# Kernel tuning notes

Measured on AMD Instinct MI355X. Metric: run time of the kernel, lower is better.

## Reference

```python
import jax, jax.numpy as jnp
import numpy as np

T, B, H, V = 128, 32, 1024, 32000


def setup_inputs() -> dict:
    key = jax.random.key(0)
    ks = jax.random.split(key, 8)
    scale = 1.0 / np.sqrt(H)
    return {
        "input": jax.random.normal(ks[0], (T, B, H), dtype=jnp.float32),
        "hidden": jnp.zeros((B, H), dtype=jnp.float32),
        "w_ic": jax.random.uniform(ks[1], (H, H), jnp.float32, -scale, scale),
        "w_ix": jax.random.uniform(ks[2], (H, H), jnp.float32, -scale, scale),
        "w_fc": jax.random.uniform(ks[3], (H, H), jnp.float32, -scale, scale),
        "w_fx": jax.random.uniform(ks[4], (H, H), jnp.float32, -scale, scale),
        "b_i": jnp.zeros((H,), dtype=jnp.float32),
        "b_f": jnp.zeros((H,), dtype=jnp.float32),
        "W_out": jax.random.uniform(ks[5], (V, H), jnp.float32, -scale, scale),
        "b_out": jnp.zeros((V,), dtype=jnp.float32),
    }


def reference(input, hidden, w_ic, w_ix, w_fc, w_fx, b_i, b_f, W_out, b_out):
    # Precompute input projections for all timesteps: [T, B, H]
    ix = jnp.einsum("tbh,kh->tbk", input, w_ix)
    fx = jnp.einsum("tbh,kh->tbk", input, w_fx)

    def step(c, xs):
        ix_t, fx_t, x_t = xs
        i_t = jax.nn.sigmoid(c @ w_ic.T + b_i + ix_t)
        f_t = jax.nn.sigmoid(c @ w_fc.T + b_f + fx_t)
        c_new = i_t * x_t + f_t * c  # RAN gated-additive update
        return c_new, c_new

    hidden_final, outputs = jax.lax.scan(step, hidden, (ix, fx, input))
    logits = jnp.einsum("tbh,vh->tbv", outputs, W_out) + b_out
    log_probs = jax.nn.log_softmax(logits, axis=-1)
    return log_probs, hidden_final
```

## Files before the change

kernel.cpp:

```cpp
#include <hip/hip_runtime.h>

typedef __attribute__((ext_vector_type(4))) float f32x4;
typedef __attribute__((ext_vector_type(8))) short bf16x8;
typedef __attribute__((ext_vector_type(4))) unsigned u32x4;

#define T_DIM 128
#define B_DIM 32
#define H_DIM 1024
#define V_DIM 32000
#define MROWS 4096
#define NBLK 64
#define CSTEP 32768
#define PUBSTEP 32768
#define WSTRIDE 1028

__device__ __forceinline__ ushort f2bf(float f){
  union { float f; unsigned u; } x; x.f = f;
  unsigned u = x.u;
  unsigned r = (u + 0x7fffu + ((u >> 16) & 1u)) >> 16;
  return (ushort)r;
}
__device__ __forceinline__ float bf2f(ushort h){
  union { unsigned u; float f; } x; x.u = ((unsigned)h) << 16;
  return x.f;
}

__device__ __forceinline__ void async_copy16(void* lds, const void* g){
  __builtin_amdgcn_global_load_lds((const __attribute__((address_space(1))) void*)g,
                                   (__attribute__((address_space(3))) void*)lds, 16, 0, 0);
}

__global__ void cast_bf16_kernel(const float* __restrict__ s, ushort* __restrict__ d, int n4){
  int stride = gridDim.x * blockDim.x;
  for (int i = blockIdx.x*blockDim.x + threadIdx.x; i < n4; i += stride){
    float4 v = ((const float4*)s)[i];
    ushort4 o = make_ushort4(f2bf(v.x), f2bf(v.y), f2bf(v.z), f2bf(v.w));
    ((ushort4*)d)[i] = o;
  }
}

__global__ void cast_split_kernel(const float* __restrict__ s, ushort* __restrict__ dh,
                                  ushort* __restrict__ dl, int n4){
  int stride = gridDim.x * blockDim.x;
  for (int i = blockIdx.x*blockDim.x + threadIdx.x; i < n4; i += stride){
    float4 v = ((const float4*)s)[i];
    ushort4 h = make_ushort4(f2bf(v.x), f2bf(v.y), f2bf(v.z), f2bf(v.w));
    ushort4 l = make_ushort4(f2bf(v.x - bf2f(h.x)), f2bf(v.y - bf2f(h.y)),
                             f2bf(v.z - bf2f(h.z)), f2bf(v.w - bf2f(h.w)));
    ((ushort4*)dh)[i] = h;
    ((ushort4*)dl)[i] = l;
  }
}

__global__ __launch_bounds__(256) void gemm_bt(
    const ushort* __restrict__ A, const ushort* __restrict__ B,
    float* __restrict__ C, const float* __restrict__ bias,
    int N, int K, int NTN, int order, int achunk,
    float* __restrict__ pmax, float* __restrict__ psum)
{
  __shared__ ushort lA[128*32];
  __shared__ ushort lB[128*32];
  __shared__ float pmS[4][64], psS[4][64];
  int tid = threadIdx.x;
  int lane = tid & 63, wid = tid >> 6;
  int bid = blockIdx.x;
  int tm, tn;
  if (order){
    int xcd = bid & 7, id = bid >> 3;
    tn = id >> 2;
    tm = (xcd << 2) | (id & 3);
  } else {
    tm = bid / NTN; tn = bid % NTN;
  }
  int row0 = tm << 7, col0 = tn << 7;

  f32x4 acc[4][4] = {};

  auto stage = [&](const ushort* __restrict__ g, ushort* l, int r0, int k0){
    int c = wid << 1;
    const ushort* s0 = g + (size_t)(r0 + (c<<4) + (lane>>2))*K + k0 + ((lane&3)<<3);
    async_copy16(l + (c<<9), s0);
    async_copy16(l + ((c+1)<<9), s0 + (size_t)16*K);
  };
  auto stageAc = [&](const ushort* __restrict__ g, ushort* l, int r0, int k0){
    int c = wid << 1;
    int cb  = (k0 >> 4) + ((lane & 3) >> 1);
    int sub = (lane & 1) << 3;
    int rA = r0 + (c<<4) + (lane>>2);
    const ushort* sA = g + ((size_t)(rA>>5)<<15) + (cb<<9) + ((rA&31)<<4) + sub;
    async_copy16(l + (c<<9), sA);
    int rB = rA + 16;
    const ushort* sB = g + ((size_t)(rB>>5)<<15) + (cb<<9) + ((rB&31)<<4) + sub;
    async_copy16(l + ((c+1)<<9), sB);
  };

  int nk = K >> 5;
  if (achunk) stageAc(A, lA, row0, 0); else stage(A, lA, row0, 0);
  stage(B, lB, col0, 0);
  int wm = (wid >> 1) << 6, wn = (wid & 1) << 6;
  int kg = (lane >> 4) << 3;
  int ar = lane & 15;

  for (int kt = 0; kt < nk; ++kt){
    __syncthreads();
    bf16x8 af[4], bfr[4];
    #pragma unroll
    for (int mi = 0; mi < 4; ++mi) af[mi]  = *(const bf16x8*)&lA[(wm + mi*16 + ar)*32 + kg];
    #pragma unroll
    for (int ni = 0; ni < 4; ++ni) bfr[ni] = *(const bf16x8*)&lB[(wn + ni*16 + ar)*32 + kg];
    #pragma unroll
    for (int mi = 0; mi < 4; ++mi)
      #pragma unroll
      for (int ni = 0; ni < 4; ++ni)
        acc[mi][ni] = __builtin_amdgcn_mfma_f32_16x16x32_bf16(af[mi], bfr[ni], acc[mi][ni], 0, 0, 0);
    if (kt + 1 < nk){
      __syncthreads();
      if (achunk) stageAc(A, lA, row0, (kt+1) << 5); else stage(A, lA, row0, (kt+1) << 5);
      stage(B, lB, col0, (kt+1) << 5);
    }
  }

  int rr = (lane >> 4) << 2;
  float bb4[4];
  #pragma unroll
  for (int ni = 0; ni < 4; ++ni) bb4[ni] = bias ? bias[col0 + wn + ni*16 + ar] : 0.f;

  #pragma unroll
  for (int mi = 0; mi < 4; ++mi){
    #pragma unroll
    for (int q = 0; q < 4; ++q){
      int r = row0 + wm + mi*16 + rr + q;
      float vals[4];
      #pragma unroll
      for (int ni = 0; ni < 4; ++ni){
        vals[ni] = acc[mi][ni][q] + bb4[ni];
        C[(size_t)r * N + col0 + wn + ni*16 + ar] = vals[ni];
      }
      if (pmax){
        float m = fmaxf(fmaxf(vals[0], vals[1]), fmaxf(vals[2], vals[3]));
        #pragma unroll
        for (int o = 1; o < 16; o <<= 1) m = fmaxf(m, __shfl_xor(m, o));
        float s = expf(vals[0]-m) + expf(vals[1]-m) + expf(vals[2]-m) + expf(vals[3]-m);
        #pragma unroll
        for (int o = 1; o < 16; o <<= 1) s += __shfl_xor(s, o);
        if (ar == 0){ int rl = mi*16 + rr + q; pmS[wid][rl] = m; psS[wid][rl] = s; }
      }
    }
  }
  if (pmax){
    __syncthreads();
    if (tid < 128){
      int rl = tid & 63, half = tid >> 6;
      int w0 = half*2, w1 = w0 + 1;
      float m0 = pmS[w0][rl], m1 = pmS[w1][rl];
      float s0 = psS[w0][rl], s1 = psS[w1][rl];
      float M = fmaxf(m0, m1);
      float S = s0*expf(m0-M) + s1*expf(m1-M);
      int r = row0 + half*64 + rl;
      pmax[(size_t)r*NTN + tn] = M;
      psum[(size_t)r*NTN + tn] = S;
    }
  }
}

__global__ __launch_bounds__(256) void gemm_bt_split(
    const ushort* __restrict__ Ah, const ushort* __restrict__ Al,
    const ushort* __restrict__ Bh, const ushort* __restrict__ Bl,
    float* __restrict__ C, int N, int K, int NTN)
{
  __shared__ ushort lAh[128*32], lAl[128*32], lBh[128*32], lBl[128*32];
  int tid = threadIdx.x;
  int lane = tid & 63, wid = tid >> 6;
  int tm = blockIdx.x / NTN, tn = blockIdx.x % NTN;
  int row0 = tm << 7, col0 = tn << 7;

  f32x4 acc[4][4] = {};

  auto stage = [&](const ushort* __restrict__ g, ushort* l, int r0, int k0){
    int c = wid << 1;
    const ushort* s0 = g + (size_t)(r0 + (c<<4) + (lane>>2))*K + k0 + ((lane&3)<<3);
    async_copy16(l + (c<<9), s0);
    async_copy16(l + ((c+1)<<9), s0 + (size_t)16*K);
  };

  int nk = K >> 5;
  stage(Ah, lAh, row0, 0); stage(Al, lAl, row0, 0);
  stage(Bh, lBh, col0, 0); stage(Bl, lBl, col0, 0);
  int wm = (wid >> 1) << 6, wn = (wid & 1) << 6;
  int kg = (lane >> 4) << 3;
  int ar = lane & 15;

  for (int kt = 0; kt < nk; ++kt){
    __syncthreads();
    bf16x8 afh[4], afl[4], bfh[4], bfl[4];
    #pragma unroll
    for (int mi = 0; mi < 4; ++mi){
      afh[mi] = *(const bf16x8*)&lAh[(wm + mi*16 + ar)*32 + kg];
      afl[mi] = *(const bf16x8*)&lAl[(wm + mi*16 + ar)*32 + kg];
    }
    #pragma unroll
    for (int ni = 0; ni < 4; ++ni){
      bfh[ni] = *(const bf16x8*)&lBh[(wn + ni*16 + ar)*32 + kg];
      bfl[ni] = *(const bf16x8*)&lBl[(wn + ni*16 + ar)*32 + kg];
    }
    #pragma unroll
    for (int mi = 0; mi < 4; ++mi)
      #pragma unroll
      for (int ni = 0; ni < 4; ++ni){
        acc[mi][ni] = __builtin_amdgcn_mfma_f32_16x16x32_bf16(afh[mi], bfh[ni], acc[mi][ni], 0, 0, 0);
        acc[mi][ni] = __builtin_amdgcn_mfma_f32_16x16x32_bf16(afh[mi], bfl[ni], acc[mi][ni], 0, 0, 0);
        acc[mi][ni] = __builtin_amdgcn_mfma_f32_16x16x32_bf16(afl[mi], bfh[ni], acc[mi][ni], 0, 0, 0);
      }
    if (kt + 1 < nk){
      __syncthreads();
      stage(Ah, lAh, row0, (kt+1) << 5); stage(Al, lAl, row0, (kt+1) << 5);
      stage(Bh, lBh, col0, (kt+1) << 5); stage(Bl, lBl, col0, (kt+1) << 5);
    }
  }

  int rr = (lane >> 4) << 2;
  #pragma unroll
  for (int mi = 0; mi < 4; ++mi)
    #pragma unroll
    for (int ni = 0; ni < 4; ++ni){
      int r  = row0 + wm + mi*16 + rr;
      int cc = col0 + wn + ni*16 + ar;
      #pragma unroll
      for (int q = 0; q < 4; ++q)
        C[(size_t)(r + q) * N + cc] = acc[mi][ni][q];
    }
}

__global__ __launch_bounds__(512) void ran_all(
    unsigned* __restrict__ pub, const float* __restrict__ hiddenf,
    const ushort* __restrict__ wh, const ushort* __restrict__ wl,
    const float* __restrict__ b_i, const float* __restrict__ b_f,
    const float* __restrict__ ixfx, const float* __restrict__ x_all,
    float* __restrict__ hid_final)
{
  __shared__ ushort lWh[32*WSTRIDE];
  __shared__ ushort lWl[32*WSTRIDE];
  __shared__ f32x4 part[4][2][2][64];
  __shared__ float gsm[2*32*17];
  __shared__ float cfl[32][17];

  int tid = threadIdx.x, lane = tid & 63, wid = tid >> 6;
  int kq = wid & 3, mh = wid >> 2;
  int rgate = wid & 1, rmh = (wid >> 1) & 1;
  int bid = blockIdx.x;
  int nb = bid << 4;
  int ar = lane & 15, kg = (lane >> 4) << 3;
  int um = tid >> 4, uk = tid & 15;

  #pragma unroll
  for (int u = 0; u < 8; ++u){
    int unit = u*512 + tid;
    int r = unit >> 7, off = (unit & 127) << 3;
    int g = r >> 4, c = r & 15;
    size_t gsrc = (size_t)((g<<10) + nb + c) * H_DIM + off;
    *(bf16x8*)&lWh[r*WSTRIDE + off] = *(const bf16x8*)&wh[gsrc];
    *(bf16x8*)&lWl[r*WSTRIDE + off] = *(const bf16x8*)&wl[gsrc];
  }
  cfl[um][uk] = hiddenf[(um<<10) + nb + uk];
  float bb = (rgate ? b_f : b_i)[nb + ar];
  const ushort* b0h = &lWh[(     ar)*WSTRIDE + (kq<<8) + kg];
  const ushort* b0l = &lWl[(     ar)*WSTRIDE + (kq<<8) + kg];
  const ushort* b1h = &lWh[(16 + ar)*WSTRIDE + (kq<<8) + kg];
  const ushort* b1l = &lWl[(16 + ar)*WSTRIDE + (kq<<8) + kg];
  int abase = (kq<<13) + ((kg>>4)<<9) + (((mh<<4) + ar)<<4) + (kg & 8);
  __syncthreads();

  for (int t = 0; t < T_DIM; ++t){
    float xq1 = x_all[((size_t)t<<15) + (um<<10) + nb + uk];
    float pix[4];
    if (wid < 4){
      const float* ix_t = ixfx + ((size_t)t<<16);
      #pragma unroll
      for (int q = 0; q < 4; ++q){
        int m = (rmh<<4) + ((lane>>4)<<2) + q;
        pix[q] = ix_t[m*2048 + (rgate<<10) + nb + ar];
      }
    }

    const unsigned* ps = pub + ((size_t)t << 15) + abase;
    unsigned expt = (unsigned)(t + 1) << 16;
    u32x4 w0[8], w1[8];
    int tries = 0;
    while (1){
      #pragma unroll
      for (int f = 0; f < 8; ++f){
        const unsigned* p = ps + (f << 10);
        asm volatile("global_load_dwordx4 %0, %2, off sc0 sc1\n\t"
                     "global_load_dwordx4 %1, %2, off offset:16 sc0 sc1"
                     : "=&v"(w0[f]), "=&v"(w1[f]) : "v"(p));
      }
      asm volatile("s_waitcnt vmcnt(0)" ::: "memory");
      __builtin_amdgcn_sched_barrier(0);
      unsigned bad = 0;
      #pragma unroll
      for (int f = 0; f < 8; ++f){
        bad |= (w0[f][0]^expt)|(w0[f][1]^expt)|(w0[f][2]^expt)|(w0[f][3]^expt)
             | (w1[f][0]^expt)|(w1[f][1]^expt)|(w1[f][2]^expt)|(w1[f][3]^expt);
      }
      if (__ballot((bad & 0xFFFF0000u) != 0) == 0ull) break;
      if (++tries > (1<<15)) break;
    }

    f32x4 g0h = {}, g0l = {}, g1h = {}, g1l = {};
    #pragma unroll
    for (int f = 0; f < 8; ++f){
      union { unsigned u[4]; bf16x8 v; } cv;
      cv.u[0] = (w0[f][0] & 0xFFFFu) | (w0[f][1] << 16);
      cv.u[1] = (w0[f][2] & 0xFFFFu) | (w0[f][3] << 16);
      cv.u[2] = (w1[f][0] & 0xFFFFu) | (w1[f][1] << 16);
      cv.u[3] = (w1[f][2] & 0xFFFFu) | (w1[f][3] << 16);
      int ob = f << 5;
      bf16x8 v0h = *(const bf16x8*)&b0h[ob];
      bf16x8 v0l = *(const bf16x8*)&b0l[ob];
      bf16x8 v1h = *(const bf16x8*)&b1h[ob];
      bf16x8 v1l = *(const bf16x8*)&b1l[ob];
      g0h = __builtin_amdgcn_mfma_f32_16x16x32_bf16(cv.v, v0h, g0h, 0, 0, 0);
      g0l = __builtin_amdgcn_mfma_f32_16x16x32_bf16(cv.v, v0l, g0l, 0, 0, 0);
      g1h = __builtin_amdgcn_mfma_f32_16x16x32_bf16(cv.v, v1h, g1h, 0, 0, 0);
      g1l = __builtin_amdgcn_mfma_f32_16x16x32_bf16(cv.v, v1l, g1l, 0, 0, 0);
    }
    part[kq][mh][0][lane] = g0h + g0l;
    part[kq][mh][1][lane] = g1h + g1l;
    __syncthreads();

    if (wid < 4){
      f32x4 sum = part[0][rmh][rgate][lane] + part[1][rmh][rgate][lane]
                + part[2][rmh][rgate][lane] + part[3][rmh][rgate][lane];
      #pragma unroll
      for (int q = 0; q < 4; ++q){
        int m = (rmh<<4) + ((lane>>4)<<2) + q;
        float pre = sum[q] + bb + pix[q];
        gsm[((rgate<<5) + m)*17 + ar] = 1.f / (1.f + expf(-pre));
      }
    }
    __syncthreads();

    {
      float iv = gsm[um*17 + uk];
      float fv = gsm[(32+um)*17 + uk];
      float cv2 = cfl[um][uk];
      float cn = iv * xq1 + fv * cv2;
      cfl[um][uk] = cn;
      unsigned word = ((unsigned)(t + 2) << 16) | (unsigned)f2bf(cn);
      __hip_atomic_store(&pub[((size_t)(t+1) << 15) + (bid << 9) + tid], word,
                         __ATOMIC_RELAXED, __HIP_MEMORY_SCOPE_AGENT);
      if (t == T_DIM-1) hid_final[(um<<10) + nb + uk] = cn;
    }
    __syncthreads();
  }
}

__global__ void init_c_kernel(const float* __restrict__ hidden, unsigned* __restrict__ pub){
  int i = blockIdx.x * blockDim.x + threadIdx.x;
  float v = hidden[i];
  int m = i >> 10, col = i & 1023;
  pub[((col>>4)<<9) + (m<<4) + (col&15)] = (1u << 16) | (unsigned)f2bf(v);
}

__global__ void untag_kernel(const unsigned* __restrict__ pub, ushort* __restrict__ cst){
  int e = (blockIdx.x * blockDim.x + threadIdx.x) << 2;
  int s = e >> 15, w = e & 32767;
  const unsigned* p = pub + ((size_t)(s + 1) << 15) + w;
  ushort4 o = make_ushort4((ushort)p[0], (ushort)p[1], (ushort)p[2], (ushort)p[3]);
  *(ushort4*)&cst[e] = o;
}

__global__ __launch_bounds__(64) void lse_reduce(const float* __restrict__ pmax,
                                                 const float* __restrict__ psum,
                                                 float* __restrict__ lse, int ntn){
  int row = blockIdx.x, lane = threadIdx.x;
  float m = -1e30f, s = 0.f;
  for (int i = lane; i < ntn; i += 64){
    float mi = pmax[(size_t)row*ntn + i], si = psum[(size_t)row*ntn + i];
    float M = fmaxf(m, mi);
    s = s*expf(m - M) + si*expf(mi - M);
    m = M;
  }
  #pragma unroll
  for (int o = 32; o; o >>= 1){
    float m2 = __shfl_xor(m, o), s2 = __shfl_xor(s, o);
    float M = fmaxf(m, m2);
    s = s*expf(m - M) + s2*expf(m2 - M);
    m = M;
  }
  if (lane == 0) lse[row] = m + logf(s);
}

__global__ __launch_bounds__(256) void sub_kernel(float* __restrict__ logits,
                                                  const float* __restrict__ lse){
  size_t row = blockIdx.x;
  float l = lse[row];
  float4* p4 = (float4*)(logits + row * (size_t)V_DIM);
  for (int i = threadIdx.x; i < V_DIM/4; i += 256){
    float4 v = p4[i];
    v.x -= l; v.y -= l; v.z -= l; v.w -= l;
    p4[i] = v;
  }
}

extern "C" void kernel_launch(void* const* d_in, const int* in_sizes, int n_in,
                              void* d_out, int out_size, void* d_ws, size_t ws_size,
                              hipStream_t stream)
{
  const float* input  = (const float*)d_in[0];
  const float* hidden = (const float*)d_in[1];
  const float* w_ic   = (const float*)d_in[2];
  const float* w_ix   = (const float*)d_in[3];
  const float* w_fc   = (const float*)d_in[4];
  const float* w_fx   = (const float*)d_in[5];
  const float* b_i    = (const float*)d_in[6];
  const float* b_f    = (const float*)d_in[7];
  const float* W_out  = (const float*)d_in[8];
  const float* b_out  = (const float*)d_in[9];
  float* out = (float*)d_out;

  char* ws = (char*)d_ws;
  ushort* wout_bf = (ushort*)(ws + 0);
  ushort* in_hi   = (ushort*)(ws + 65536000);
  ushort* in_lo   = (ushort*)(ws + 73924608);
  ushort* wx_hi   = (ushort*)(ws + 82313216);
  ushort* wx_lo   = (ushort*)(ws + 86507520);
  ushort* wc_hi   = (ushort*)(ws + 90701824);
  ushort* wc_lo   = (ushort*)(ws + 94896128);
  unsigned* pub   = (unsigned*)(ws + 65536000);
  ushort* cstate  = (ushort*)(ws + 82444288);
  float*  pmax    = (float*)(ws + 94896128);
  float*  psum    = (float*)(ws + 99090432);
  float*  lse     = (float*)(ws + 103186432);
  float*  ixfx    = out;

  cast_bf16_kernel <<<2048,256,0,stream>>>(W_out, wout_bf, V_DIM*H_DIM/4);
  cast_split_kernel<<<1024,256,0,stream>>>(input, in_hi, in_lo, MROWS*H_DIM/4);
  cast_split_kernel<<<256,256,0,stream>>>(w_ix, wx_hi,             wx_lo,             H_DIM*H_DIM/4);
  cast_split_kernel<<<256,256,0,stream>>>(w_fx, wx_hi+H_DIM*H_DIM, wx_lo+H_DIM*H_DIM, H_DIM*H_DIM/4);
  cast_split_kernel<<<256,256,0,stream>>>(w_ic, wc_hi,             wc_lo,             H_DIM*H_DIM/4);
  cast_split_kernel<<<256,256,0,stream>>>(w_fc, wc_hi+H_DIM*H_DIM, wc_lo+H_DIM*H_DIM, H_DIM*H_DIM/4);

  gemm_bt_split<<<32*16,256,0,stream>>>(in_hi, in_lo, wx_hi, wx_lo, ixfx, 2048, H_DIM, 16);

  hipMemsetAsync(pub, 0, (size_t)129 * PUBSTEP * 4, stream);
  init_c_kernel<<<128,256,0,stream>>>(hidden, pub);

  ran_all<<<NBLK,512,0,stream>>>(pub, hidden, wc_hi, wc_lo, b_i, b_f,
                                 ixfx, input, out + (size_t)MROWS*V_DIM);

  untag_kernel<<<4096,256,0,stream>>>(pub, cstate);
  gemm_bt<<<32*250,256,0,stream>>>(cstate, wout_bf, out, b_out, V_DIM, H_DIM, 250, 1, 1, pmax, psum);
  lse_reduce<<<MROWS,64,0,stream>>>(pmax, psum, lse, 250);
  sub_kernel<<<MROWS,256,0,stream>>>(out, lse);
}
```

Baseline: 1.999 ms.

## Replace output projection GEMM with 256x256 double-buffered swizzled LDS kernel

The vocabulary projection GEMM moves from 128x128 tiles with single-buffered K=32 stages to 256x256 tiles with 512 threads, K=64 stages, double-buffered async LDS loads, and XOR-swizzled LDS layout to avoid bank conflicts. This raises arithmetic intensity per byte loaded and overlaps global loads with MFMA work. The partial softmax max/sum is reduced across four column waves, and the LSE reduction now covers 125 partials. The larger tile uses much more LDS (about 128KB), which limits occupancy to one block per CU. Tile edges depend on V being divisible by 256, which holds for 32000.

```diff
diff --git a/kernel.cpp b/kernel.cpp
--- a/kernel.cpp
+++ b/kernel.cpp
@@ -10,7 +10,6 @@
 #define V_DIM 32000
 #define MROWS 4096
 #define NBLK 64
-#define CSTEP 32768
 #define PUBSTEP 32768
 #define WSTRIDE 1028
 
@@ -52,114 +51,119 @@
   }
 }
 
-__global__ __launch_bounds__(256) void gemm_bt(
+__global__ __launch_bounds__(512) void gemm256(
     const ushort* __restrict__ A, const ushort* __restrict__ B,
     float* __restrict__ C, const float* __restrict__ bias,
-    int N, int K, int NTN, int order, int achunk,
     float* __restrict__ pmax, float* __restrict__ psum)
 {
-  __shared__ ushort lA[128*32];
-  __shared__ ushort lB[128*32];
-  __shared__ float pmS[4][64], psS[4][64];
-  int tid = threadIdx.x;
-  int lane = tid & 63, wid = tid >> 6;
+  __shared__ ushort lA[2][256*64];
+  __shared__ ushort lB[2][256*64];
+  __shared__ float redm[2][4][128], reds[2][4][128];
+
+  const int K = 1024, N = V_DIM, NTN = 125, NT = 16;
+  int tid = threadIdx.x, lane = tid & 63, wid = tid >> 6;
+  int wm = wid >> 2, wn = wid & 3;
   int bid = blockIdx.x;
-  int tm, tn;
-  if (order){
-    int xcd = bid & 7, id = bid >> 3;
-    tn = id >> 2;
-    tm = (xcd << 2) | (id & 3);
-  } else {
-    tm = bid / NTN; tn = bid % NTN;
-  }
-  int row0 = tm << 7, col0 = tn << 7;
-
-  f32x4 acc[4][4] = {};
-
-  auto stage = [&](const ushort* __restrict__ g, ushort* l, int r0, int k0){
-    int c = wid << 1;
-    const ushort* s0 = g + (size_t)(r0 + (c<<4) + (lane>>2))*K + k0 + ((lane&3)<<3);
-    async_copy16(l + (c<<9), s0);
-    async_copy16(l + ((c+1)<<9), s0 + (size_t)16*K);
+  int xcd = bid & 7, id = bid >> 3;
+  int tm = (xcd << 1) | (id & 1);
+  int tn = id >> 1;
+  int row0 = tm << 8, col0 = tn << 8;
+  int ar = lane & 15, kg = (lane >> 4) << 3;
+
+  auto STAGE = [&](int buf, int k0){
+    #pragma unroll
+    for (int j = 0; j < 4; ++j){
+      int l16 = j*512 + tid;
+      int row = l16 >> 3, g = l16 & 7;
+      int kc = (g ^ (row & 7)) << 3;
+      int rA = row0 + row, k = k0 + kc;
+      const ushort* sA = A + ((size_t)(rA>>5)<<15) + ((k>>4)<<9) + ((rA&31)<<4) + (k&15);
+      async_copy16(&lA[buf][l16<<3], sA);
+    }
+    #pragma unroll
+    for (int j = 0; j < 4; ++j){
+      int l16 = j*512 + tid;
+      int row = l16 >> 3, g = l16 & 7;
+      int kc = (g ^ (row & 7)) << 3;
+      const ushort* sB = B + (size_t)(col0 + row)*K + k0 + kc;
+      async_copy16(&lB[buf][l16<<3], sB);
+    }
   };
-  auto stageAc = [&](const ushort* __restrict__ g, ushort* l, int r0, int k0){
-    int c = wid << 1;
-    int cb  = (k0 >> 4) + ((lane & 3) >> 1);
-    int sub = (lane & 1) << 3;
-    int rA = r0 + (c<<4) + (lane>>2);
-    const ushort* sA = g + ((size_t)(rA>>5)<<15) + (cb<<9) + ((rA&31)<<4) + sub;
-    async_copy16(l + (c<<9), sA);
-    int rB = rA + 16;
-    const ushort* sB = g + ((size_t)(rB>>5)<<15) + (cb<<9) + ((rB&31)<<4) + sub;
-    async_copy16(l + ((c+1)<<9), sB);
-  };
-
-  int nk = K >> 5;
-  if (achunk) stageAc(A, lA, row0, 0); else stage(A, lA, row0, 0);
-  stage(B, lB, col0, 0);
-  int wm = (wid >> 1) << 6, wn = (wid & 1) << 6;
-  int kg = (lane >> 4) << 3;
-  int ar = lane & 15;
-
-  for (int kt = 0; kt < nk; ++kt){
-    __syncthreads();
-    bf16x8 af[4], bfr[4];
-    #pragma unroll
-    for (int mi = 0; mi < 4; ++mi) af[mi]  = *(const bf16x8*)&lA[(wm + mi*16 + ar)*32 + kg];
-    #pragma unroll
-    for (int ni = 0; ni < 4; ++ni) bfr[ni] = *(const bf16x8*)&lB[(wn + ni*16 + ar)*32 + kg];
-    #pragma unroll
-    for (int mi = 0; mi < 4; ++mi)
-      #pragma unroll
-      for (int ni = 0; ni < 4; ++ni)
-        acc[mi][ni] = __builtin_amdgcn_mfma_f32_16x16x32_bf16(af[mi], bfr[ni], acc[mi][ni], 0, 0, 0);
-    if (kt + 1 < nk){
-      __syncthreads();
-      if (achunk) stageAc(A, lA, row0, (kt+1) << 5); else stage(A, lA, row0, (kt+1) << 5);
-      stage(B, lB, col0, (kt+1) << 5);
-    }
-  }
-
-  int rr = (lane >> 4) << 2;
+
+  f32x4 acc[8][4] = {};
+
+  STAGE(0, 0);
+  for (int t = 0; t < NT; ++t){
+    if (t + 1 < NT) STAGE((t+1) & 1, (t+1) << 6);
+    if (t + 1 < NT) asm volatile("s_waitcnt vmcnt(8)" ::: "memory");
+    else            asm volatile("s_waitcnt vmcnt(0)" ::: "memory");
+    __builtin_amdgcn_s_barrier();
+    __builtin_amdgcn_sched_barrier(0);
+    const ushort* bufA = lA[t & 1];
+    const ushort* bufB = lB[t & 1];
+    #pragma unroll
+    for (int ks = 0; ks < 2; ++ks){
+      bf16x8 a[8], b[4];
+      #pragma unroll
+      for (int fr = 0; fr < 8; ++fr){
+        int row = wm*128 + fr*16 + ar;
+        int gk = ks*4 + (kg >> 3);
+        a[fr] = *(const bf16x8*)&bufA[row*64 + ((gk ^ (row & 7)) << 3)];
+      }
+      #pragma unroll
+      for (int fc = 0; fc < 4; ++fc){
+        int row = wn*64 + fc*16 + ar;
+        int gk = ks*4 + (kg >> 3);
+        b[fc] = *(const bf16x8*)&bufB[row*64 + ((gk ^ (row & 7)) << 3)];
+      }
+      __builtin_amdgcn_s_setprio(1);
+      #pragma unroll
+      for (int fr = 0; fr < 8; ++fr)
+        #pragma unroll
+        for (int fc = 0; fc < 4; ++fc)
+          acc[fr][fc] = __builtin_amdgcn_mfma_f32_16x16x32_bf16(a[fr], b[fc], acc[fr][fc], 0, 0, 0);
+      __builtin_amdgcn_s_setprio(0);
+    }
+    __builtin_amdgcn_sched_barrier(0);
+    __builtin_amdgcn_s_barrier();
+    __builtin_amdgcn_sched_barrier(0);
+  }
+
   float bb4[4];
   #pragma unroll
-  for (int ni = 0; ni < 4; ++ni) bb4[ni] = bias ? bias[col0 + wn + ni*16 + ar] : 0.f;
-
+  for (int fc = 0; fc < 4; ++fc) bb4[fc] = bias[col0 + wn*64 + fc*16 + ar];
   #pragma unroll
-  for (int mi = 0; mi < 4; ++mi){
+  for (int fr = 0; fr < 8; ++fr){
     #pragma unroll
     for (int q = 0; q < 4; ++q){
-      int r = row0 + wm + mi*16 + rr + q;
+      int rl = fr*16 + (lane>>4)*4 + q;
+      int r = row0 + wm*128 + rl;
       float vals[4];
       #pragma unroll
-      for (int ni = 0; ni < 4; ++ni){
-        vals[ni] = acc[mi][ni][q] + bb4[ni];
-        C[(size_t)r * N + col0 + wn + ni*16 + ar] = vals[ni];
-      }
-      if (pmax){
-        float m = fmaxf(fmaxf(vals[0], vals[1]), fmaxf(vals[2], vals[3]));
-        #pragma unroll
-        for (int o = 1; o < 16; o <<= 1) m = fmaxf(m, __shfl_xor(m, o));
-        float s = expf(vals[0]-m) + expf(vals[1]-m) + expf(vals[2]-m) + expf(vals[3]-m);
-        #pragma unroll
-        for (int o = 1; o < 16; o <<= 1) s += __shfl_xor(s, o);
-        if (ar == 0){ int rl = mi*16 + rr + q; pmS[wid][rl] = m; psS[wid][rl] = s; }
-      }
-    }
-  }
-  if (pmax){
-    __syncthreads();
-    if (tid < 128){
-      int rl = tid & 63, half = tid >> 6;
-      int w0 = half*2, w1 = w0 + 1;
-      float m0 = pmS[w0][rl], m1 = pmS[w1][rl];
-      float s0 = psS[w0][rl], s1 = psS[w1][rl];
-      float M = fmaxf(m0, m1);
-      float S = s0*expf(m0-M) + s1*expf(m1-M);
-      int r = row0 + half*64 + rl;
-      pmax[(size_t)r*NTN + tn] = M;
-      psum[(size_t)r*NTN + tn] = S;
-    }
+      for (int fc = 0; fc < 4; ++fc){
+        vals[fc] = acc[fr][fc][q] + bb4[fc];
+        C[(size_t)r * N + col0 + wn*64 + fc*16 + ar] = vals[fc];
+      }
+      float m = fmaxf(fmaxf(vals[0], vals[1]), fmaxf(vals[2], vals[3]));
+      #pragma unroll
+      for (int o = 1; o < 16; o <<= 1) m = fmaxf(m, __shfl_xor(m, o));
+      float s = expf(vals[0]-m) + expf(vals[1]-m) + expf(vals[2]-m) + expf(vals[3]-m);
+      #pragma unroll
+      for (int o = 1; o < 16; o <<= 1) s += __shfl_xor(s, o);
+      if (ar == 0){ redm[wm][wn][rl] = m; reds[wm][wn][rl] = s; }
+    }
+  }
+  __syncthreads();
+  if (tid < 256){
+    int wm2 = tid >> 7, rl = tid & 127;
+    float m0 = redm[wm2][0][rl], m1 = redm[wm2][1][rl];
+    float m2 = redm[wm2][2][rl], m3 = redm[wm2][3][rl];
+    float M = fmaxf(fmaxf(m0, m1), fmaxf(m2, m3));
+    float S = reds[wm2][0][rl]*expf(m0-M) + reds[wm2][1][rl]*expf(m1-M)
+            + reds[wm2][2][rl]*expf(m2-M) + reds[wm2][3][rl]*expf(m3-M);
+    int r = row0 + wm2*128 + rl;
+    pmax[(size_t)r*NTN + tn] = M;
+    psum[(size_t)r*NTN + tn] = S;
   }
 }
 
@@ -450,7 +454,7 @@
                                  ixfx, input, out + (size_t)MROWS*V_DIM);
 
   untag_kernel<<<4096,256,0,stream>>>(pub, cstate);
-  gemm_bt<<<32*250,256,0,stream>>>(cstate, wout_bf, out, b_out, V_DIM, H_DIM, 250, 1, 1, pmax, psum);
-  lse_reduce<<<MROWS,64,0,stream>>>(pmax, psum, lse, 250);
+  gemm256<<<2000,512,0,stream>>>(cstate, wout_bf, out, b_out, pmax, psum);
+  lse_reduce<<<MROWS,64,0,stream>>>(pmax, psum, lse, 125);
   sub_kernel<<<MROWS,256,0,stream>>>(out, lse);
 }
```

Result: faster. 1.915 ms (-4.2%).
